# Kernel optimization log

Hardware: AMD Instinct MI355X
Metric: run time of the kernel (lower is better)

The kernel has to match this reference:

```python
import jax, jax.numpy as jnp
from jax import lax
import numpy as np

K_UP = 5
SCALE = 2


def _cbs(x, w, s, b, groups=1):
    # yolov5 Conv: conv2d(bias=False, pad=k//2) + BN(eval, folded into scale/bias) + SiLU
    y = lax.conv_general_dilated(x, w, (1, 1), 'SAME',
                                 dimension_numbers=('NCHW', 'OIHW', 'NCHW'),
                                 feature_group_count=groups)
    y = y * s[None, :, None, None] + b[None, :, None, None]
    return y * jax.nn.sigmoid(y)


def _msgconv(x, p):
    (cv1_w, cv1_s, cv1_b, dw3_w, dw3_s, dw3_b,
     dw5_w, dw5_s, dw5_b, px_w, px_s, px_b) = p
    x1 = _cbs(x, cv1_w, cv1_s, cv1_b)                      # [b, min_ch, h, w]
    ch = x1.shape[1] // 2
    # rearrange 'bs (g ch) h w -> bs ch h w g' with g=2: group0=ch[:half], group1=ch[half:]
    g0 = _cbs(x1[:, :ch], dw3_w, dw3_s, dw3_b, groups=ch)  # depthwise k=3
    g1 = _cbs(x1[:, ch:], dw5_w, dw5_s, dw5_b, groups=ch)  # depthwise k=5
    x2 = jnp.concatenate([g0, g1], axis=1)
    return _cbs(jnp.concatenate([x1, x2], axis=1), px_w, px_s, px_b)


def _carafe(X, comp_p, enc_p):
    b, c, h, w = X.shape
    r, k = SCALE, K_UP
    k2 = k * k
    W = _msgconv(_msgconv(X, comp_p), enc_p)               # [b, (r*k)^2, h, w]
    # PixelShuffle(r): [b, k2*r^2, h, w] -> [b, k2, h*r, w*r]
    W = W.reshape(b, k2, r, r, h, w).transpose(0, 1, 4, 2, 5, 3).reshape(b, k2, h * r, w * r)
    W = jax.nn.softmax(W, axis=1)
    # nearest upsample by r
    Xu = jnp.repeat(jnp.repeat(X, r, axis=2), r, axis=3)   # [b, c, h_, w_]
    h_, w_ = h * r, w * r
    pad = (k // 2) * r                                      # 4
    Xp = jnp.pad(Xu, ((0, 0), (0, 0), (pad, pad), (pad, pad)))
    # Unfold(kernel=k, dilation=r, padding=pad): kernel pos (p,q) -> offset r*p, r*q in padded map
    patches = jnp.stack([Xp[:, :, r * p:r * p + h_, r * q:r * q + w_]
                         for p in range(k) for q in range(k)], axis=2)  # [b, c, k2, h_, w_]
    return jnp.einsum('bkhw,bckhw->bchw', W, patches)


def _conv_params(key, cout, cin, k):
    k1, k2, k3 = jax.random.split(key, 3)
    w = jax.random.normal(k1, (cout, cin, k, k), jnp.float32) / np.float32(np.sqrt(cin * k * k))
    s = 1.0 + 0.1 * jax.random.normal(k2, (cout,), jnp.float32)
    b = 0.1 * jax.random.normal(k3, (cout,), jnp.float32)
    return w, s, b


def setup_inputs() -> dict:
    key = jax.random.key(0)
    ks = jax.random.split(key, 9)
    c, c_mid = 128, 64
    enc_out = (SCALE * K_UP) ** 2  # 100
    d = {'X': jax.random.normal(ks[0], (2, c, 64, 64), jnp.float32)}
    mc = c_mid // 2                # 32
    d['comp_cv1_w'], d['comp_cv1_s'], d['comp_cv1_b'] = _conv_params(ks[1], mc, c, 1)
    d['comp_dw3_w'], d['comp_dw3_s'], d['comp_dw3_b'] = _conv_params(ks[2], mc // 2, 1, 3)
    d['comp_dw5_w'], d['comp_dw5_s'], d['comp_dw5_b'] = _conv_params(ks[3], mc // 2, 1, 5)
    d['comp_px_w'], d['comp_px_s'], d['comp_px_b'] = _conv_params(ks[4], c_mid, c_mid, 1)
    me = enc_out // 2              # 50
    d['enc_cv1_w'], d['enc_cv1_s'], d['enc_cv1_b'] = _conv_params(ks[5], me, c_mid, 1)
    d['enc_dw3_w'], d['enc_dw3_s'], d['enc_dw3_b'] = _conv_params(ks[6], me // 2, 1, 3)
    d['enc_dw5_w'], d['enc_dw5_s'], d['enc_dw5_b'] = _conv_params(ks[7], me // 2, 1, 5)
    d['enc_px_w'], d['enc_px_s'], d['enc_px_b'] = _conv_params(ks[8], enc_out, enc_out, 1)
    return d


def reference(X, comp_cv1_w, comp_cv1_s, comp_cv1_b, comp_dw3_w, comp_dw3_s, comp_dw3_b,
              comp_dw5_w, comp_dw5_s, comp_dw5_b, comp_px_w, comp_px_s, comp_px_b,
              enc_cv1_w, enc_cv1_s, enc_cv1_b, enc_dw3_w, enc_dw3_s, enc_dw3_b,
              enc_dw5_w, enc_dw5_s, enc_dw5_b, enc_px_w, enc_px_s, enc_px_b):
    comp_p = (comp_cv1_w, comp_cv1_s, comp_cv1_b, comp_dw3_w, comp_dw3_s, comp_dw3_b,
              comp_dw5_w, comp_dw5_s, comp_dw5_b, comp_px_w, comp_px_s, comp_px_b)
    enc_p = (enc_cv1_w, enc_cv1_s, enc_cv1_b, enc_dw3_w, enc_dw3_s, enc_dw3_b,
             enc_dw5_w, enc_dw5_s, enc_dw5_b, enc_px_w, enc_px_s, enc_px_b)
    return _carafe(X, comp_p, enc_p)
```

## Files before the change

### kernel.cpp

```cpp
#include <hip/hip_runtime.h>
#include <math.h>

__device__ __forceinline__ float silu_act(float y) {
    return y / (1.f + __expf(-y));
}

template<int TC, int CIN>
__global__ void pw_conv_silu(const float* __restrict__ in, int HW, int B,
                             const float* __restrict__ w,
                             const float* __restrict__ sc, const float* __restrict__ bi,
                             float* __restrict__ out, int CoutStride) {
    int g = blockIdx.x * blockDim.x + threadIdx.x;
    if (g >= B * HW) return;
    int b = g / HW, pix = g - b * HW;
    int co0 = blockIdx.y * TC;
    float acc[TC];
#pragma unroll
    for (int j = 0; j < TC; ++j) acc[j] = 0.f;
    const float* ip = in + (size_t)b * CIN * HW + pix;
    const float* wp = w + (size_t)co0 * CIN;
#pragma unroll 8
    for (int ci = 0; ci < CIN; ++ci) {
        float v = ip[(size_t)ci * HW];
#pragma unroll
        for (int j = 0; j < TC; ++j)
            acc[j] = fmaf(v, wp[j * CIN + ci], acc[j]);
    }
#pragma unroll
    for (int j = 0; j < TC; ++j) {
        int co = co0 + j;
        float y = fmaf(acc[j], sc[co], bi[co]);
        out[((size_t)b * CoutStride + co) * HW + pix] = silu_act(y);
    }
}

__global__ void dw_conv_silu(float* __restrict__ cat, int ch, int H, int W, int Ctot, int B,
                             const float* __restrict__ w3, const float* __restrict__ s3,
                             const float* __restrict__ b3,
                             const float* __restrict__ w5, const float* __restrict__ s5,
                             const float* __restrict__ b5) {
    int HW = H * W;
    int idx = blockIdx.x * blockDim.x + threadIdx.x;
    int total = B * 2 * ch * HW;
    if (idx >= total) return;
    int pix = idx % HW;
    int t = idx / HW;
    int c2 = t % (2 * ch);
    int b = t / (2 * ch);
    int x = pix % W, y = pix / W;
    const float* ip = cat + ((size_t)b * Ctot + c2) * HW;
    float acc = 0.f, scale, bias;
    if (c2 < ch) {
        const float* wk = w3 + c2 * 9;
#pragma unroll
        for (int ky = 0; ky < 3; ++ky) {
            int iy = y + ky - 1;
            if ((unsigned)iy >= (unsigned)H) continue;
#pragma unroll
            for (int kx = 0; kx < 3; ++kx) {
                int ix = x + kx - 1;
                if ((unsigned)ix >= (unsigned)W) continue;
                acc = fmaf(ip[iy * W + ix], wk[ky * 3 + kx], acc);
            }
        }
        scale = s3[c2]; bias = b3[c2];
    } else {
        int c = c2 - ch;
        const float* wk = w5 + c * 25;
#pragma unroll
        for (int ky = 0; ky < 5; ++ky) {
            int iy = y + ky - 2;
            if ((unsigned)iy >= (unsigned)H) continue;
#pragma unroll
            for (int kx = 0; kx < 5; ++kx) {
                int ix = x + kx - 2;
                if ((unsigned)ix >= (unsigned)W) continue;
                acc = fmaf(ip[iy * W + ix], wk[ky * 5 + kx], acc);
            }
        }
        scale = s5[c]; bias = b5[c];
    }
    float v = fmaf(acc, scale, bias);
    cat[((size_t)b * Ctot + 2 * ch + c2) * HW + pix] = silu_act(v);
}

__global__ __launch_bounds__(256) void carafe_kernel(
        const float* __restrict__ X, const float* __restrict__ wraw,
        float* __restrict__ out) {
    const int H = 64, Wd = 64, C = 128, Ho = 128, Wo = 128, HW = H * Wd;
    int Y = blockIdx.x;
    int cchunk = blockIdx.y;
    int b = blockIdx.z;
    __shared__ float xs[16][5][68];
    int t = threadIdx.x;
    int c0 = cchunk * 16;
    const float* Xb = X + ((size_t)b * C + c0) * HW;
    for (int i = t; i < 16 * 5 * 68; i += 256) {
        int col = i % 68;
        int tmp = i / 68;
        int p = tmp % 5;
        int c = tmp / 5;
        int iy = Y + p - 2;
        int ix = col - 2;
        float v = 0.f;
        if ((unsigned)iy < (unsigned)H && (unsigned)ix < (unsigned)Wd)
            v = Xb[(size_t)c * HW + iy * Wd + ix];
        xs[c][p][col] = v;
    }
    int l = t & 63;
    int tc = t >> 6;
    const float* wb = wraw + (size_t)b * 100 * HW + Y * Wd + l;
    float wreg[4][25];
#pragma unroll
    for (int rp = 0; rp < 4; ++rp)
#pragma unroll
        for (int j = 0; j < 25; ++j)
            wreg[rp][j] = wb[(size_t)(j * 4 + rp) * HW];
#pragma unroll
    for (int rp = 0; rp < 4; ++rp) {
        float m = -1e30f;
#pragma unroll
        for (int j = 0; j < 25; ++j) m = fmaxf(m, wreg[rp][j]);
        float s = 0.f;
#pragma unroll
        for (int j = 0; j < 25; ++j) { wreg[rp][j] = __expf(wreg[rp][j] - m); s += wreg[rp][j]; }
        float inv = 1.f / s;
#pragma unroll
        for (int j = 0; j < 25; ++j) wreg[rp][j] *= inv;
    }
    __syncthreads();

#pragma unroll
    for (int k = 0; k < 4; ++k) {
        int c = tc * 4 + k;
        float a00 = 0.f, a01 = 0.f, a10 = 0.f, a11 = 0.f;
#pragma unroll
        for (int p = 0; p < 5; ++p)
#pragma unroll
            for (int q = 0; q < 5; ++q) {
                float v = xs[c][p][l + q];
                int j = p * 5 + q;
                a00 = fmaf(wreg[0][j], v, a00);
                a01 = fmaf(wreg[1][j], v, a01);
                a10 = fmaf(wreg[2][j], v, a10);
                a11 = fmaf(wreg[3][j], v, a11);
            }
        size_t ob = (((size_t)b * C + (c0 + c)) * Ho + 2 * Y) * Wo + 2 * l;
        *reinterpret_cast<float2*>(&out[ob])      = make_float2(a00, a01);
        *reinterpret_cast<float2*>(&out[ob + Wo]) = make_float2(a10, a11);
    }
}

extern "C" void kernel_launch(void* const* d_in, const int* in_sizes, int n_in,
                              void* d_out, int out_size, void* d_ws, size_t ws_size,
                              hipStream_t stream) {
    const float* X          = (const float*)d_in[0];
    const float* comp_cv1_w = (const float*)d_in[1];
    const float* comp_cv1_s = (const float*)d_in[2];
    const float* comp_cv1_b = (const float*)d_in[3];
    const float* comp_dw3_w = (const float*)d_in[4];
    const float* comp_dw3_s = (const float*)d_in[5];
    const float* comp_dw3_b = (const float*)d_in[6];
    const float* comp_dw5_w = (const float*)d_in[7];
    const float* comp_dw5_s = (const float*)d_in[8];
    const float* comp_dw5_b = (const float*)d_in[9];
    const float* comp_px_w  = (const float*)d_in[10];
    const float* comp_px_s  = (const float*)d_in[11];
    const float* comp_px_b  = (const float*)d_in[12];
    const float* enc_cv1_w  = (const float*)d_in[13];
    const float* enc_cv1_s  = (const float*)d_in[14];
    const float* enc_cv1_b  = (const float*)d_in[15];
    const float* enc_dw3_w  = (const float*)d_in[16];
    const float* enc_dw3_s  = (const float*)d_in[17];
    const float* enc_dw3_b  = (const float*)d_in[18];
    const float* enc_dw5_w  = (const float*)d_in[19];
    const float* enc_dw5_s  = (const float*)d_in[20];
    const float* enc_dw5_b  = (const float*)d_in[21];
    const float* enc_px_w   = (const float*)d_in[22];
    const float* enc_px_s   = (const float*)d_in[23];
    const float* enc_px_b   = (const float*)d_in[24];
    float* out = (float*)d_out;

    const int B = 2, H = 64, W = 64, HW = H * W;
    float* cat_c  = (float*)d_ws;
    float* y_comp = cat_c  + (size_t)B * 64 * HW;
    float* cat_e  = y_comp + (size_t)B * 64 * HW;
    float* wraw   = cat_e  + (size_t)B * 100 * HW;

    int pixBlocks = (B * HW + 255) / 256;

    pw_conv_silu<4, 128><<<dim3(pixBlocks, 8), 256, 0, stream>>>(
        X, HW, B, comp_cv1_w, comp_cv1_s, comp_cv1_b, cat_c, 64);
    {
        int n = B * 32 * HW;
        dw_conv_silu<<<(n + 255) / 256, 256, 0, stream>>>(
            cat_c, 16, H, W, 64, B,
            comp_dw3_w, comp_dw3_s, comp_dw3_b,
            comp_dw5_w, comp_dw5_s, comp_dw5_b);
    }
    pw_conv_silu<4, 64><<<dim3(pixBlocks, 16), 256, 0, stream>>>(
        cat_c, HW, B, comp_px_w, comp_px_s, comp_px_b, y_comp, 64);

    pw_conv_silu<5, 64><<<dim3(pixBlocks, 10), 256, 0, stream>>>(
        y_comp, HW, B, enc_cv1_w, enc_cv1_s, enc_cv1_b, cat_e, 100);
    {
        int n = B * 50 * HW;
        dw_conv_silu<<<(n + 255) / 256, 256, 0, stream>>>(
            cat_e, 25, H, W, 100, B,
            enc_dw3_w, enc_dw3_s, enc_dw3_b,
            enc_dw5_w, enc_dw5_s, enc_dw5_b);
    }
    pw_conv_silu<5, 100><<<dim3(pixBlocks, 20), 256, 0, stream>>>(
        cat_e, HW, B, enc_px_w, enc_px_s, enc_px_b, wraw, 100);

    carafe_kernel<<<dim3(64, 8, B), 256, 0, stream>>>(X, wraw, out);
}
```

Measured before the change: 78.85 us.

## Fuse comp depthwise convs and pointwise projection into one row-tiled kernel

Replaces the compressor stage's separate depthwise-conv kernel and pointwise-projection kernel with a single kernel. Each block handles one image row: it computes the 3x3/5x5 depthwise outputs, stages them together with the x1 row in shared memory, then does the 64->64 pointwise conv from LDS. This removes one launch and the global write/read of the concatenated intermediate. In exchange, each output-group block (4 per row) recomputes the depthwise convs, and the grid is smaller (512 blocks).

```diff
diff --git a/kernel.cpp b/kernel.cpp
--- a/kernel.cpp
+++ b/kernel.cpp
@@ -84,6 +84,77 @@
     cat[((size_t)b * Ctot + 2 * ch + c2) * HW + pix] = silu_act(v);
 }
 
+__global__ __launch_bounds__(256) void fusedA_kernel(
+        const float* __restrict__ x1c,
+        const float* __restrict__ w3, const float* __restrict__ s3, const float* __restrict__ b3,
+        const float* __restrict__ w5, const float* __restrict__ s5, const float* __restrict__ b5,
+        const float* __restrict__ pxw, const float* __restrict__ pxs, const float* __restrict__ pxb,
+        float* __restrict__ y) {
+    const int H = 64, Wd = 64, HW = 4096;
+    int Y = blockIdx.x, og = blockIdx.y, b = blockIdx.z;
+    __shared__ float cat[64][64];
+    int t = threadIdx.x;
+    int l = t & 63;
+    int w = __builtin_amdgcn_readfirstlane(t >> 6);
+    const float* src = x1c + (size_t)b * 32 * HW;
+#pragma unroll
+    for (int k = 0; k < 8; ++k) {
+        int c = w + 4 * k;
+        const float* ip = src + (size_t)c * HW;
+        float acc = 0.f, sc, bi;
+        if (c < 16) {
+            const float* wk = w3 + c * 9;
+#pragma unroll
+            for (int p = 0; p < 3; ++p) {
+                int iy = Y + p - 1;
+                if ((unsigned)iy >= (unsigned)H) continue;
+#pragma unroll
+                for (int kx = 0; kx < 3; ++kx) {
+                    int ix = l + kx - 1;
+                    if ((unsigned)ix >= (unsigned)Wd) continue;
+                    acc = fmaf(ip[iy * Wd + ix], wk[p * 3 + kx], acc);
+                }
+            }
+            sc = s3[c]; bi = b3[c];
+        } else {
+            const float* wk = w5 + (c - 16) * 25;
+#pragma unroll
+            for (int p = 0; p < 5; ++p) {
+                int iy = Y + p - 2;
+                if ((unsigned)iy >= (unsigned)H) continue;
+#pragma unroll
+                for (int kx = 0; kx < 5; ++kx) {
+                    int ix = l + kx - 2;
+                    if ((unsigned)ix >= (unsigned)Wd) continue;
+                    acc = fmaf(ip[iy * Wd + ix], wk[p * 5 + kx], acc);
+                }
+            }
+            sc = s5[c - 16]; bi = b5[c - 16];
+        }
+        cat[c][l] = ip[Y * Wd + l];
+        cat[32 + c][l] = silu_act(fmaf(acc, sc, bi));
+    }
+    __syncthreads();
+    {
+        int co0 = og * 16 + w * 4;
+        const float* wp = pxw + (size_t)co0 * 64;
+        float acc[4] = {0.f, 0.f, 0.f, 0.f};
+#pragma unroll 8
+        for (int ci = 0; ci < 64; ++ci) {
+            float xv = cat[ci][l];
+#pragma unroll
+            for (int k = 0; k < 4; ++k)
+                acc[k] = fmaf(xv, wp[k * 64 + ci], acc[k]);
+        }
+#pragma unroll
+        for (int k = 0; k < 4; ++k) {
+            int co = co0 + k;
+            y[((size_t)b * 64 + co) * HW + Y * Wd + l] =
+                silu_act(fmaf(acc[k], pxs[co], pxb[co]));
+        }
+    }
+}
+
 __global__ __launch_bounds__(256) void carafe_kernel(
         const float* __restrict__ X, const float* __restrict__ wraw,
         float* __restrict__ out) {
@@ -100,8 +171,7 @@
         int tmp = i / 68;
         int p = tmp % 5;
         int c = tmp / 5;
-        int iy = Y + p - 2;
-        int ix = col - 2;
+        int iy = Y + p - 2, ix = col - 2;
         float v = 0.f;
         if ((unsigned)iy < (unsigned)H && (unsigned)ix < (unsigned)Wd)
             v = Xb[(size_t)c * HW + iy * Wd + ix];
@@ -182,27 +252,26 @@
     float* out = (float*)d_out;
 
     const int B = 2, H = 64, W = 64, HW = H * W;
-    float* cat_c  = (float*)d_ws;
-    float* y_comp = cat_c  + (size_t)B * 64 * HW;
-    float* cat_e  = y_comp + (size_t)B * 64 * HW;
-    float* wraw   = cat_e  + (size_t)B * 100 * HW;
+    float* x1c   = (float*)d_ws;
+    float* yc    = x1c   + (size_t)B * 32 * HW;
+    float* cat_e = yc    + (size_t)B * 64 * HW;
+    float* wraw  = cat_e + (size_t)B * 100 * HW;
 
     int pixBlocks = (B * HW + 255) / 256;
 
     pw_conv_silu<4, 128><<<dim3(pixBlocks, 8), 256, 0, stream>>>(
-        X, HW, B, comp_cv1_w, comp_cv1_s, comp_cv1_b, cat_c, 64);
-    {
-        int n = B * 32 * HW;
-        dw_conv_silu<<<(n + 255) / 256, 256, 0, stream>>>(
-            cat_c, 16, H, W, 64, B,
-            comp_dw3_w, comp_dw3_s, comp_dw3_b,
-            comp_dw5_w, comp_dw5_s, comp_dw5_b);
-    }
-    pw_conv_silu<4, 64><<<dim3(pixBlocks, 16), 256, 0, stream>>>(
-        cat_c, HW, B, comp_px_w, comp_px_s, comp_px_b, y_comp, 64);
+        X, HW, B, comp_cv1_w, comp_cv1_s, comp_cv1_b, x1c, 32);
+
+    fusedA_kernel<<<dim3(64, 4, B), 256, 0, stream>>>(
+        x1c,
+        comp_dw3_w, comp_dw3_s, comp_dw3_b,
+        comp_dw5_w, comp_dw5_s, comp_dw5_b,
+        comp_px_w, comp_px_s, comp_px_b,
+        yc);
 
     pw_conv_silu<5, 64><<<dim3(pixBlocks, 10), 256, 0, stream>>>(
-        y_comp, HW, B, enc_cv1_w, enc_cv1_s, enc_cv1_b, cat_e, 100);
+        yc, HW, B, enc_cv1_w, enc_cv1_s, enc_cv1_b, cat_e, 100);
+
     {
         int n = B * 50 * HW;
         dw_conv_silu<<<(n + 255) / 256, 256, 0, stream>>>(
@@ -210,6 +279,7 @@
             enc_dw3_w, enc_dw3_s, enc_dw3_b,
             enc_dw5_w, enc_dw5_s, enc_dw5_b);
     }
+
     pw_conv_silu<5, 100><<<dim3(pixBlocks, 20), 256, 0, stream>>>(
         cat_e, HW, B, enc_px_w, enc_px_s, enc_px_b, wraw, 100);
 
```

Result: slower. 92.26 us (+17.0%).
